# Kernel optimization log

Hardware: AMD Instinct MI355X
Metric: run time of the kernel (lower is better)

## Reference

```python
import jax, jax.numpy as jnp
import numpy as np
from jax import lax

EPS = 1e-10

def _safe_norm(x):
    # torch remove_zeros: replace exact-zero norms with 1e-10
    n = jnp.linalg.norm(x, axis=-1, keepdims=True)
    return jnp.where(n != 0, n, jnp.full_like(n, EPS))

def setup_inputs() -> dict:
    key = jax.random.key(0)
    ks = jax.random.split(key, 5)
    S, B, D = 2048, 32, 512  # seq, batch, 2*hidden
    K = 147  # odd(max_entries/14)
    return {
        "encoder_outputs": jax.random.normal(ks[0], (S, B, D), dtype=jnp.float32),
        "state": jax.random.normal(ks[1], (B, D), dtype=jnp.float32),
        "previous_attention": jax.random.uniform(ks[2], (B, S), dtype=jnp.float32),
        "W_att": jax.random.normal(ks[3], (D, D), dtype=jnp.float32) / np.sqrt(D),
        "b_att": jax.random.normal(ks[4], (D,), dtype=jnp.float32) * 0.01,
        "conv_w": jnp.ones((1, 1, K), dtype=jnp.float32),
        "conv_b": jnp.zeros((1,), dtype=jnp.float32),
    }

def reference(encoder_outputs, state, previous_attention, W_att, b_att, conv_w, conv_b):
    S, B, D = encoder_outputs.shape
    # attended state via linear layer, then cosine-similarity weights (vectorized over seq)
    attended = state @ W_att.T + b_att                       # [B, D]
    ns = attended / _safe_norm(attended)                     # [B, D]
    ne = encoder_outputs / _safe_norm(encoder_outputs)       # [S, B, D]
    weights = jnp.einsum('bd,sbd->bs', ns, ne)               # [B, S]
    # conv1d time smoothing of previous attention (same-length, odd kernel)
    k = conv_w.shape[-1]
    pad = k // 2
    y = lax.conv_general_dilated(previous_attention[:, None, :], conv_w,
                                 window_strides=(1,), padding=[(pad, pad)])
    adjusted = jax.nn.relu(y[:, 0, :] + conv_b)              # [B, S]
    prev_probs = adjusted / jnp.sum(adjusted, axis=1, keepdims=True)
    adj = prev_probs * jax.nn.softmax(weights, axis=1)
    norm_w = adj / jnp.sum(adj, axis=1, keepdims=True)       # [B, S]
    applied = jnp.einsum('bs,sbd->bd', norm_w, encoder_outputs)  # [B, D]
    return applied, norm_w
```

## Files before the change

### kernel.cpp

```cpp
#include <hip/hip_runtime.h>
#include <math.h>


__device__ __forceinline__ float wave_sum(float v) {
    for (int off = 32; off; off >>= 1) v += __shfl_xor(v, off);
    return v;
}

__global__ __launch_bounds__(256) void front_kernel(
    const float* __restrict__ state, const float* __restrict__ W,
    const float* __restrict__ bias, const float* __restrict__ prev,
    const float* __restrict__ cw, const float* __restrict__ cb,
    float* __restrict__ attended, float* __restrict__ adj,
    int S, int D, int K) {
    __shared__ __align__(16) float smem[1024];
    int b = blockIdx.y;
    int t = threadIdx.x;

    if (blockIdx.x < 2) {
        if (t < D / 4)
            ((float4*)smem)[t] = ((const float4*)(state + (size_t)b * D))[t];
        __syncthreads();
        int d = blockIdx.x * 256 + t;
        const float4* Wrow = (const float4*)(W + (size_t)d * D);
        const float4* sv = (const float4*)smem;
        float acc = bias[d];
#pragma unroll 8
        for (int k = 0; k < 128; ++k) {
            float4 w4 = Wrow[k];
            float4 s4 = sv[k];
            acc += w4.x * s4.x + w4.y * s4.y + w4.z * s4.z + w4.w * s4.w;
        }
        attended[(size_t)b * D + d] = acc;
    } else {
        int s0 = (blockIdx.x - 2) * 256;
        int pad = K / 2;
        int seglen = 256 + K - 1;
        float* seg = smem;
        float* wk = smem + 512;
        for (int i = t; i < seglen; i += 256) {
            int s = s0 - pad + i;
            seg[i] = (s >= 0 && s < S) ? prev[(size_t)b * S + s] : 0.f;
        }
        for (int j = t; j < K; j += 256) wk[j] = cw[j];
        __syncthreads();
        float y = cb[0];
        for (int j = 0; j < K; ++j) y += seg[t + j] * wk[j];
        adj[(size_t)b * S + s0 + t] = fmaxf(y, 0.f);
    }
}

__global__ __launch_bounds__(256) void main_kernel(
    const float* __restrict__ e, const float* __restrict__ attended,
    const float* __restrict__ adj, float* __restrict__ partial,
    float* __restrict__ zbuf, float* __restrict__ u,
    int S, int B, int D) {
    constexpr int CH = 8;
    __shared__ __align__(16) float reds[4 * 512 + 4];
    int wave = threadIdx.x >> 6;
    int lane = threadIdx.x & 63;
    int c = blockIdx.x * 4 + wave;
    int b = blockIdx.y;

    const float4* att4 = (const float4*)(attended + (size_t)b * D);
    float4 a0 = att4[lane];
    float4 a1 = att4[lane + 64];
    float asq = a0.x * a0.x + a0.y * a0.y + a0.z * a0.z + a0.w * a0.w
              + a1.x * a1.x + a1.y * a1.y + a1.z * a1.z + a1.w * a1.w;
    asq = wave_sum(asq);
    float an = sqrtf(asq);
    if (an == 0.f) an = 1e-10f;
    float ainv = 1.f / an;
    float4 ns0, ns1;
    ns0.x = a0.x * ainv; ns0.y = a0.y * ainv; ns0.z = a0.z * ainv; ns0.w = a0.w * ainv;
    ns1.x = a1.x * ainv; ns1.y = a1.y * ainv; ns1.z = a1.z * ainv; ns1.w = a1.w * ainv;

    int s0 = c * CH;

    float adjv = (lane < CH) ? adj[(size_t)b * S + s0 + lane] : 0.f;

    float4 acc0 = {0.f, 0.f, 0.f, 0.f};
    float4 acc1 = {0.f, 0.f, 0.f, 0.f};
    float z = 0.f;

    const float4* row4 = (const float4*)(e + ((size_t)s0 * B + b) * D);
    size_t rstride = (size_t)B * D / 4;

#pragma unroll 2
    for (int i = 0; i < CH; i += 2) {
        float4 xa0 = row4[lane];
        float4 xa1 = row4[lane + 64];
        float4 xb0 = row4[rstride + lane];
        float4 xb1 = row4[rstride + lane + 64];
        float ava = __shfl(adjv, i);
        float avb = __shfl(adjv, i + 1);
        float dota = xa0.x * ns0.x + xa0.y * ns0.y + xa0.z * ns0.z + xa0.w * ns0.w
                   + xa1.x * ns1.x + xa1.y * ns1.y + xa1.z * ns1.z + xa1.w * ns1.w;
        float sqa  = xa0.x * xa0.x + xa0.y * xa0.y + xa0.z * xa0.z + xa0.w * xa0.w
                   + xa1.x * xa1.x + xa1.y * xa1.y + xa1.z * xa1.z + xa1.w * xa1.w;
        float dotb = xb0.x * ns0.x + xb0.y * ns0.y + xb0.z * ns0.z + xb0.w * ns0.w
                   + xb1.x * ns1.x + xb1.y * ns1.y + xb1.z * ns1.z + xb1.w * ns1.w;
        float sqb  = xb0.x * xb0.x + xb0.y * xb0.y + xb0.z * xb0.z + xb0.w * xb0.w
                   + xb1.x * xb1.x + xb1.y * xb1.y + xb1.z * xb1.z + xb1.w * xb1.w;
#pragma unroll
        for (int off = 32; off; off >>= 1) {
            dota += __shfl_xor(dota, off);
            dotb += __shfl_xor(dotb, off);
            sqa  += __shfl_xor(sqa, off);
            sqb  += __shfl_xor(sqb, off);
        }
        float ra = (sqa > 0.f) ? __builtin_amdgcn_rsqf(sqa) : 0.f;
        float rb = (sqb > 0.f) ? __builtin_amdgcn_rsqf(sqb) : 0.f;
        float coefa = ava * __expf(dota * ra);
        float coefb = avb * __expf(dotb * rb);
        if (lane == 0)
            *((float2*)(u + (size_t)b * S + s0 + i)) = make_float2(coefa, coefb);
        acc0.x += coefa * xa0.x + coefb * xb0.x;
        acc0.y += coefa * xa0.y + coefb * xb0.y;
        acc0.z += coefa * xa0.z + coefb * xb0.z;
        acc0.w += coefa * xa0.w + coefb * xb0.w;
        acc1.x += coefa * xa1.x + coefb * xb1.x;
        acc1.y += coefa * xa1.y + coefb * xb1.y;
        acc1.z += coefa * xa1.z + coefb * xb1.z;
        acc1.w += coefa * xa1.w + coefb * xb1.w;
        z += coefa + coefb;
        row4 += 2 * rstride;
    }

    float* wsl = reds + (wave << 9);
    ((float4*)wsl)[lane] = acc0;
    ((float4*)wsl)[lane + 64] = acc1;
    if (lane == 0) reds[2048 + wave] = z;
    __syncthreads();
    int t = threadIdx.x;
    if (t < 128) {
        const float4* r4 = (const float4*)reds;
        float4 v0 = r4[t];
        float4 v1 = r4[t + 128];
        float4 v2 = r4[t + 256];
        float4 v3 = r4[t + 384];
        float4 o;
        o.x = v0.x + v1.x + v2.x + v3.x;
        o.y = v0.y + v1.y + v2.y + v3.y;
        o.z = v0.z + v1.z + v2.z + v3.z;
        o.w = v0.w + v1.w + v2.w + v3.w;
        ((float4*)(partial + ((size_t)blockIdx.x * B + b) * D))[t] = o;
    }
    if (t == 0)
        zbuf[(size_t)blockIdx.x * B + b] =
            reds[2048] + reds[2049] + reds[2050] + reds[2051];
}

__global__ __launch_bounds__(256) void combine_kernel(
    const float* __restrict__ partial, const float* __restrict__ zbuf,
    const float* __restrict__ u, float* __restrict__ applied,
    float* __restrict__ norm_w, int S, int B, int D, int NPART) {
    int q = blockIdx.x;
    int b = blockIdx.y;
    int t = threadIdx.x;
    __shared__ __align__(16) float4 red4[8][32];
    __shared__ float zsh;

    float zt = (t < NPART) ? zbuf[(size_t)t * B + b] : 0.f;
    zt = wave_sum(zt);
    if (t == 0) zsh = 1.f / zt;

    int c2 = t >> 5;
    int di = t & 31;
    int d4 = q * 32 + di;
    const float4* p4 = (const float4*)partial;
    float4 a = {0.f, 0.f, 0.f, 0.f};
    for (int cix = c2; cix < NPART; cix += 8) {
        float4 x = p4[((size_t)cix * B + b) * (D >> 2) + d4];
        a.x += x.x; a.y += x.y; a.z += x.z; a.w += x.w;
    }
    red4[c2][di] = a;
    __syncthreads();
    float inv = zsh;
    if (t < 32) {
        float4 s = red4[0][t];
#pragma unroll
        for (int j = 1; j < 8; ++j) {
            float4 x = red4[j][t];
            s.x += x.x; s.y += x.y; s.z += x.z; s.w += x.w;
        }
        s.x *= inv; s.y *= inv; s.z *= inv; s.w *= inv;
        ((float4*)(applied + (size_t)b * D))[q * 32 + t] = s;
    }

    const float4* u4 = (const float4*)(u + (size_t)b * S);
    float4* nw4 = (float4*)(norm_w + (size_t)b * S);
    if (t < 128) {
        int idx = q * (S >> 4) + t;
        float4 x = u4[idx];
        x.x *= inv; x.y *= inv; x.z *= inv; x.w *= inv;
        nw4[idx] = x;
    }
}

extern "C" void kernel_launch(void* const* d_in, const int* in_sizes, int n_in,
                              void* d_out, int out_size, void* d_ws, size_t ws_size,
                              hipStream_t stream) {
    const float* enc   = (const float*)d_in[0];
    const float* state = (const float*)d_in[1];
    const float* prev  = (const float*)d_in[2];
    const float* W     = (const float*)d_in[3];
    const float* bias  = (const float*)d_in[4];
    const float* cw    = (const float*)d_in[5];
    const float* cb    = (const float*)d_in[6];

    const int S = in_sizes[0] / in_sizes[1];
    const int B = in_sizes[2] / S;
    const int D = in_sizes[1] / B;
    const int K = in_sizes[5];

    float* out     = (float*)d_out;
    float* applied = out;
    float* norm_w  = out + (size_t)B * D;

    const int CH = 8;
    const int NPART = S / (4 * CH);

    float* ws       = (float*)d_ws;
    float* attended = ws;
    float* adj      = attended + (size_t)B * D;
    float* u        = adj + (size_t)B * S;
    float* zbuf     = u + (size_t)B * S;
    float* partial  = zbuf + (size_t)NPART * B;

    front_kernel<<<dim3(2 + S / 256, B), 256, 0, stream>>>(
        state, W, bias, prev, cw, cb, attended, adj, S, D, K);
    main_kernel<<<dim3(NPART, B), 256, 0, stream>>>(
        enc, attended, adj, partial, zbuf, u, S, B, D);
    combine_kernel<<<dim3(4, B), 256, 0, stream>>>(
        partial, zbuf, u, applied, norm_w, S, B, D, NPART);
}
```

Baseline: 221.7 us.

## Remap main kernel waves to batches and precompute normalized state in front kernel

The main kernel now gives each wave of a block a different batch row at the same sequence chunk, so the four waves read adjacent rows of the encoder tensor. The per-block shared-memory reduction is dropped and each wave writes its own partial, which makes the partial buffer four times larger and gives combine_kernel four times more partials to sum. The attended-state normalization moves into front_kernel, which computes both halves of a row in one block, so main_kernel only loads a precomputed normalized vector. Combine_kernel now reduces z over all four waves, since NPART can exceed 64.

```diff
diff --git a/kernel.cpp b/kernel.cpp
--- a/kernel.cpp
+++ b/kernel.cpp
@@ -11,29 +11,41 @@
     const float* __restrict__ state, const float* __restrict__ W,
     const float* __restrict__ bias, const float* __restrict__ prev,
     const float* __restrict__ cw, const float* __restrict__ cb,
-    float* __restrict__ attended, float* __restrict__ adj,
+    float* __restrict__ ns, float* __restrict__ adj,
     int S, int D, int K) {
     __shared__ __align__(16) float smem[1024];
+    __shared__ float red[4];
     int b = blockIdx.y;
     int t = threadIdx.x;
-
-    if (blockIdx.x < 2) {
+    int lane = t & 63, wv = t >> 6;
+
+    if (blockIdx.x == 0) {
         if (t < D / 4)
             ((float4*)smem)[t] = ((const float4*)(state + (size_t)b * D))[t];
         __syncthreads();
-        int d = blockIdx.x * 256 + t;
-        const float4* Wrow = (const float4*)(W + (size_t)d * D);
         const float4* sv = (const float4*)smem;
-        float acc = bias[d];
+        float acc0 = bias[t];
+        float acc1 = bias[t + 256];
+        const float4* W0 = (const float4*)(W + (size_t)t * D);
+        const float4* W1 = (const float4*)(W + (size_t)(t + 256) * D);
 #pragma unroll 8
         for (int k = 0; k < 128; ++k) {
-            float4 w4 = Wrow[k];
             float4 s4 = sv[k];
-            acc += w4.x * s4.x + w4.y * s4.y + w4.z * s4.z + w4.w * s4.w;
-        }
-        attended[(size_t)b * D + d] = acc;
+            float4 w0 = W0[k];
+            float4 w1 = W1[k];
+            acc0 += w0.x * s4.x + w0.y * s4.y + w0.z * s4.z + w0.w * s4.w;
+            acc1 += w1.x * s4.x + w1.y * s4.y + w1.z * s4.z + w1.w * s4.w;
+        }
+        float sq = acc0 * acc0 + acc1 * acc1;
+        sq = wave_sum(sq);
+        if (lane == 0) red[wv] = sq;
+        __syncthreads();
+        float tot = red[0] + red[1] + red[2] + red[3];
+        float inv = (tot > 0.f) ? __builtin_amdgcn_rsqf(tot) : 0.f;
+        ns[(size_t)b * D + t] = acc0 * inv;
+        ns[(size_t)b * D + t + 256] = acc1 * inv;
     } else {
-        int s0 = (blockIdx.x - 2) * 256;
+        int s0 = (blockIdx.x - 1) * 256;
         int pad = K / 2;
         int seglen = 256 + K - 1;
         float* seg = smem;
@@ -51,31 +63,20 @@
 }
 
 __global__ __launch_bounds__(256) void main_kernel(
-    const float* __restrict__ e, const float* __restrict__ attended,
+    const float* __restrict__ e, const float* __restrict__ ns,
     const float* __restrict__ adj, float* __restrict__ partial,
     float* __restrict__ zbuf, float* __restrict__ u,
     int S, int B, int D) {
     constexpr int CH = 8;
-    __shared__ __align__(16) float reds[4 * 512 + 4];
     int wave = threadIdx.x >> 6;
     int lane = threadIdx.x & 63;
-    int c = blockIdx.x * 4 + wave;
-    int b = blockIdx.y;
-
-    const float4* att4 = (const float4*)(attended + (size_t)b * D);
-    float4 a0 = att4[lane];
-    float4 a1 = att4[lane + 64];
-    float asq = a0.x * a0.x + a0.y * a0.y + a0.z * a0.z + a0.w * a0.w
-              + a1.x * a1.x + a1.y * a1.y + a1.z * a1.z + a1.w * a1.w;
-    asq = wave_sum(asq);
-    float an = sqrtf(asq);
-    if (an == 0.f) an = 1e-10f;
-    float ainv = 1.f / an;
-    float4 ns0, ns1;
-    ns0.x = a0.x * ainv; ns0.y = a0.y * ainv; ns0.z = a0.z * ainv; ns0.w = a0.w * ainv;
-    ns1.x = a1.x * ainv; ns1.y = a1.y * ainv; ns1.z = a1.z * ainv; ns1.w = a1.w * ainv;
-
-    int s0 = c * CH;
+    int b = blockIdx.y * 4 + wave;
+    int sx = blockIdx.x;
+    int s0 = sx * CH;
+
+    const float4* ns4 = (const float4*)(ns + (size_t)b * D);
+    float4 ns0 = ns4[lane];
+    float4 ns1 = ns4[lane + 64];
 
     float adjv = (lane < CH) ? adj[(size_t)b * S + s0 + lane] : 0.f;
 
@@ -127,28 +128,10 @@
         row4 += 2 * rstride;
     }
 
-    float* wsl = reds + (wave << 9);
-    ((float4*)wsl)[lane] = acc0;
-    ((float4*)wsl)[lane + 64] = acc1;
-    if (lane == 0) reds[2048 + wave] = z;
-    __syncthreads();
-    int t = threadIdx.x;
-    if (t < 128) {
-        const float4* r4 = (const float4*)reds;
-        float4 v0 = r4[t];
-        float4 v1 = r4[t + 128];
-        float4 v2 = r4[t + 256];
-        float4 v3 = r4[t + 384];
-        float4 o;
-        o.x = v0.x + v1.x + v2.x + v3.x;
-        o.y = v0.y + v1.y + v2.y + v3.y;
-        o.z = v0.z + v1.z + v2.z + v3.z;
-        o.w = v0.w + v1.w + v2.w + v3.w;
-        ((float4*)(partial + ((size_t)blockIdx.x * B + b) * D))[t] = o;
-    }
-    if (t == 0)
-        zbuf[(size_t)blockIdx.x * B + b] =
-            reds[2048] + reds[2049] + reds[2050] + reds[2051];
+    float4* p4 = (float4*)(partial + ((size_t)sx * B + b) * D);
+    p4[lane] = acc0;
+    p4[lane + 64] = acc1;
+    if (lane == 0) zbuf[(size_t)sx * B + b] = z;
 }
 
 __global__ __launch_bounds__(256) void combine_kernel(
@@ -159,11 +142,12 @@
     int b = blockIdx.y;
     int t = threadIdx.x;
     __shared__ __align__(16) float4 red4[8][32];
+    __shared__ float zred[4];
     __shared__ float zsh;
 
     float zt = (t < NPART) ? zbuf[(size_t)t * B + b] : 0.f;
     zt = wave_sum(zt);
-    if (t == 0) zsh = 1.f / zt;
+    if ((t & 63) == 0) zred[t >> 6] = zt;
 
     int c2 = t >> 5;
     int di = t & 31;
@@ -175,6 +159,8 @@
         a.x += x.x; a.y += x.y; a.z += x.z; a.w += x.w;
     }
     red4[c2][di] = a;
+    __syncthreads();
+    if (t == 0) zsh = 1.f / (zred[0] + zred[1] + zred[2] + zred[3]);
     __syncthreads();
     float inv = zsh;
     if (t < 32) {
@@ -219,19 +205,19 @@
     float* norm_w  = out + (size_t)B * D;
 
     const int CH = 8;
-    const int NPART = S / (4 * CH);
+    const int NPART = S / CH;
 
     float* ws       = (float*)d_ws;
-    float* attended = ws;
-    float* adj      = attended + (size_t)B * D;
+    float* nsbuf    = ws;
+    float* adj      = nsbuf + (size_t)B * D;
     float* u        = adj + (size_t)B * S;
     float* zbuf     = u + (size_t)B * S;
     float* partial  = zbuf + (size_t)NPART * B;
 
-    front_kernel<<<dim3(2 + S / 256, B), 256, 0, stream>>>(
-        state, W, bias, prev, cw, cb, attended, adj, S, D, K);
-    main_kernel<<<dim3(NPART, B), 256, 0, stream>>>(
-        enc, attended, adj, partial, zbuf, u, S, B, D);
+    front_kernel<<<dim3(1 + S / 256, B), 256, 0, stream>>>(
+        state, W, bias, prev, cw, cb, nsbuf, adj, S, D, K);
+    main_kernel<<<dim3(S / CH, B / 4), 256, 0, stream>>>(
+        enc, nsbuf, adj, partial, zbuf, u, S, B, D);
     combine_kernel<<<dim3(4, B), 256, 0, stream>>>(
         partial, zbuf, u, applied, norm_w, S, B, D, NPART);
 }
```

Result: slower. 250.1 us (+12.8%).
